# Performance work log

Measured on AMD Instinct MI355X. Metric: run time of the kernel, lower is better.

## Reference

```python
import jax, jax.numpy as jnp
import numpy as np

B, TQ, TK = 8, 256, 256
DQ, DK, DV, H = 512, 512, 512, 256


def setup_inputs() -> dict:
    key = jax.random.key(0)
    k1, k2, k3, k4, k5, k6 = jax.random.split(key, 6)
    queries = jax.random.normal(k1, (B, TQ, DQ), dtype=jnp.float32)
    keys = jax.random.normal(k2, (B, TK, DK), dtype=jnp.float32)
    values = jax.random.normal(k3, (B, TK, DV), dtype=jnp.float32)
    # Linear(in, out, bias=False): y = x @ W.T with W (out,in); store transposed (in,out)
    Wq = jax.random.normal(k4, (DQ, H), dtype=jnp.float32) / np.sqrt(DQ)
    Wk = jax.random.normal(k5, (DK, H), dtype=jnp.float32) / np.sqrt(DK)
    wv = jax.random.normal(k6, (H,), dtype=jnp.float32) / np.sqrt(H)
    return {"queries": queries, "keys": keys, "values": values,
            "Wq": Wq, "Wk": Wk, "wv": wv}


def reference(queries, keys, values, Wq, Wk, wv):
    q = jnp.einsum('bqd,dh->bqh', queries, Wq)          # (B,Tq,H)
    k = jnp.einsum('bkd,dh->bkh', keys, Wk)             # (B,Tk,H)
    features = jnp.tanh(q[:, :, None, :] + k[:, None, :, :])  # (B,Tq,Tk,H)
    scores = jnp.einsum('bqkh,h->bqk', features, wv)    # (B,Tq,Tk)
    attn = jax.nn.softmax(scores, axis=-1)              # (B,Tq,Tk)
    return jnp.einsum('bqk,bkv->bqv', attn, values)     # (B,Tq,Dv)
```

## Files before the change

### kernel.cpp

```cpp
#include <hip/hip_runtime.h>

typedef float v2f __attribute__((ext_vector_type(2)));
typedef short bf16x8 __attribute__((ext_vector_type(8)));
typedef float f32x4 __attribute__((ext_vector_type(4)));

namespace {
constexpr int B   = 8;
constexpr int TQ  = 256;
constexpr int TK  = 256;
constexpr int DQK = 512;
constexpr int DV  = 512;
constexpr int H   = 256;
constexpr int QB  = 4;
constexpr float C2LOG2E   = 2.8853900817779268f;
constexpr float NEG2LOG2E = -2.8853900817779268f;
}

__device__ __forceinline__ uint32_t f2u(float x) { return __builtin_bit_cast(uint32_t, x); }
__device__ __forceinline__ float u2f(uint32_t x) { return __builtin_bit_cast(float, x); }
__device__ __forceinline__ uint32_t pack_hi(float x, float y) {
    return (f2u(y) & 0xFFFF0000u) | (f2u(x) >> 16);
}

__global__ __launch_bounds__(256)
void proj_kernel(const float* __restrict__ Q, const float* __restrict__ Kin,
                 const float* __restrict__ Wq, const float* __restrict__ Wk,
                 float* __restrict__ qpc, float* __restrict__ kpc4)
{
    __shared__ short Ahi[4][64][8];
    __shared__ short Alo[4][64][8];
    __shared__ short Bhi[4][32][8];
    __shared__ short Blo[4][32][8];

    const bool kside = (blockIdx.z == 1);
    const float* A = kside ? Kin : Q;
    const float* W = kside ? Wk  : Wq;
    const int m0 = blockIdx.x * 64;
    const int n0 = blockIdx.y * 32;
    const int tid = threadIdx.x;

    const int am = tid >> 2, ag = tid & 3;
    const int bk = tid >> 3, bn4 = (tid & 7) * 4;
    const float4* aptr = (const float4*)(A + (m0 + am) * DQK) + ag * 2;
    const float*  wptr = W + bk * H + n0 + bn4;

    const int w = tid >> 6, l = tid & 63;
    const int wm = (w >> 1) * 32, wn = (w & 1) * 16;
    const int fg = l >> 4;
    const int fr = l & 15;

    float4 a0 = aptr[0], a1 = aptr[1];
    float4 bv = *(const float4*)wptr;

    f32x4 acc0 = {0.f, 0.f, 0.f, 0.f};
    f32x4 acc1 = {0.f, 0.f, 0.f, 0.f};

    for (int s = 0; s < 16; ++s) {
        __syncthreads();
        {
            float ah0 = u2f(f2u(a0.x) & 0xFFFF0000u), ah1 = u2f(f2u(a0.y) & 0xFFFF0000u);
            float ah2 = u2f(f2u(a0.z) & 0xFFFF0000u), ah3 = u2f(f2u(a0.w) & 0xFFFF0000u);
            float ah4 = u2f(f2u(a1.x) & 0xFFFF0000u), ah5 = u2f(f2u(a1.y) & 0xFFFF0000u);
            float ah6 = u2f(f2u(a1.z) & 0xFFFF0000u), ah7 = u2f(f2u(a1.w) & 0xFFFF0000u);
            int4 hw, lw;
            hw.x = (int)pack_hi(a0.x, a0.y); hw.y = (int)pack_hi(a0.z, a0.w);
            hw.z = (int)pack_hi(a1.x, a1.y); hw.w = (int)pack_hi(a1.z, a1.w);
            lw.x = (int)pack_hi(a0.x - ah0, a0.y - ah1);
            lw.y = (int)pack_hi(a0.z - ah2, a0.w - ah3);
            lw.z = (int)pack_hi(a1.x - ah4, a1.y - ah5);
            lw.w = (int)pack_hi(a1.z - ah6, a1.w - ah7);
            *(int4*)&Ahi[ag][am][0] = hw;
            *(int4*)&Alo[ag][am][0] = lw;
            const int g = bk >> 3, slot = bk & 7;
            float bb[4] = {bv.x, bv.y, bv.z, bv.w};
            #pragma unroll
            for (int i = 0; i < 4; ++i) {
                uint32_t u = f2u(bb[i]);
                float hf = u2f(u & 0xFFFF0000u);
                Bhi[g][bn4 + i][slot] = (short)(u >> 16);
                Blo[g][bn4 + i][slot] = (short)(f2u(bb[i] - hf) >> 16);
            }
        }
        __syncthreads();
        if (s < 15) {
            a0 = aptr[s * 8 + 8];
            a1 = aptr[s * 8 + 9];
            bv = *(const float4*)(wptr + (s + 1) * 32 * H);
        }
        bf16x8 ah_0 = *(const bf16x8*)&Ahi[fg][wm + fr][0];
        bf16x8 ah_1 = *(const bf16x8*)&Ahi[fg][wm + 16 + fr][0];
        bf16x8 al_0 = *(const bf16x8*)&Alo[fg][wm + fr][0];
        bf16x8 al_1 = *(const bf16x8*)&Alo[fg][wm + 16 + fr][0];
        bf16x8 bh   = *(const bf16x8*)&Bhi[fg][wn + fr][0];
        bf16x8 bl   = *(const bf16x8*)&Blo[fg][wn + fr][0];
        acc0 = __builtin_amdgcn_mfma_f32_16x16x32_bf16(ah_0, bh, acc0, 0, 0, 0);
        acc1 = __builtin_amdgcn_mfma_f32_16x16x32_bf16(ah_1, bh, acc1, 0, 0, 0);
        acc0 = __builtin_amdgcn_mfma_f32_16x16x32_bf16(ah_0, bl, acc0, 0, 0, 0);
        acc1 = __builtin_amdgcn_mfma_f32_16x16x32_bf16(ah_1, bl, acc1, 0, 0, 0);
        acc0 = __builtin_amdgcn_mfma_f32_16x16x32_bf16(al_0, bh, acc0, 0, 0, 0);
        acc1 = __builtin_amdgcn_mfma_f32_16x16x32_bf16(al_1, bh, acc1, 0, 0, 0);
    }

    const int col = n0 + wn + fr;
    #pragma unroll
    for (int mi = 0; mi < 2; ++mi) {
        f32x4 acc = mi ? acc1 : acc0;
        #pragma unroll
        for (int r = 0; r < 4; ++r) {
            const int row = m0 + wm + mi * 16 + fg * 4 + r;
            float val = __builtin_amdgcn_exp2f(acc[r] * C2LOG2E);
            if (!kside) {
                qpc[row * H + col] = val;
            } else {
                const int bb2 = row >> 8, kk = row & 255;
                kpc4[((bb2 * (H / 4) + (col >> 2)) * TK + kk) * 4 + (col & 3)] = val;
            }
        }
    }
}

__global__ __launch_bounds__(512, 8)
void attn_kernel(const float* __restrict__ qpc, const float* __restrict__ kpc4,
                 const float* __restrict__ wv, const float* __restrict__ values,
                 float* __restrict__ opart, float* __restrict__ rs_g)
{
    __shared__ float qlds[H][QB];
    __shared__ float wlds[H];
    __shared__ float accbuf[8][QB][128];
    __shared__ float pT[128][QB];

    const int bid = blockIdx.x;
    const int b   = bid >> 7;
    const int qg  = (bid >> 1) & 63;
    const int kh  = bid & 1;
    const int q0  = qg * QB;
    const int tid = threadIdx.x;

    for (int i = tid; i < QB * H; i += 512) {
        const int h = i >> 2, q = i & 3;
        qlds[h][q] = qpc[(b * TQ + q0 + q) * H + h];
    }
    if (tid < H) wlds[tid] = wv[tid];
    __syncthreads();

    {
        const int kp = tid & 63;
        const int hg = tid >> 6;
        const int h0 = hg * 32;
        const float4* kc = (const float4*)kpc4 + (b * (H / 4) + hg * 8) * TK
                           + (kh * 128 + 2 * kp);
        v2f a01a = {0.f, 0.f}, a23a = {0.f, 0.f};
        v2f a01b = {0.f, 0.f}, a23b = {0.f, 0.f};
        float4 kva4 = kc[0];
        float4 kvb4 = kc[1];
        #pragma unroll
        for (int h4 = 0; h4 < 8; ++h4) {
            float4 nkva, nkvb;
            if (h4 < 7) {
                nkva = kc[(h4 + 1) * TK];
                nkvb = kc[(h4 + 1) * TK + 1];
            }
            float4 w4 = *(const float4*)&wlds[h0 + h4 * 4];
            #pragma unroll
            for (int j = 0; j < 4; ++j) {
                const int h = h0 + h4 * 4 + j;
                const float ea = (j == 0) ? kva4.x : (j == 1) ? kva4.y : (j == 2) ? kva4.z : kva4.w;
                const float eb = (j == 0) ? kvb4.x : (j == 1) ? kvb4.y : (j == 2) ? kvb4.z : kvb4.w;
                const float wj = (j == 0) ? w4.x  : (j == 1) ? w4.y  : (j == 2) ? w4.z  : w4.w;
                float4 qa = *(const float4*)&qlds[h][0];
                v2f q01 = {qa.x, qa.y}, q23 = {qa.z, qa.w};
                v2f ea2 = {ea, ea}, eb2 = {eb, eb}, w2 = {wj, wj};
                v2f one = {1.0f, 1.0f};
                v2f d0a = __builtin_elementwise_fma(q01, ea2, one);
                v2f d1a = __builtin_elementwise_fma(q23, ea2, one);
                v2f d0b = __builtin_elementwise_fma(q01, eb2, one);
                v2f d1b = __builtin_elementwise_fma(q23, eb2, one);
                v2f r0a, r1a, r0b, r1b;
                r0a.x = __builtin_amdgcn_rcpf(d0a.x);
                r0a.y = __builtin_amdgcn_rcpf(d0a.y);
                r1a.x = __builtin_amdgcn_rcpf(d1a.x);
                r1a.y = __builtin_amdgcn_rcpf(d1a.y);
                r0b.x = __builtin_amdgcn_rcpf(d0b.x);
                r0b.y = __builtin_amdgcn_rcpf(d0b.y);
                r1b.x = __builtin_amdgcn_rcpf(d1b.x);
                r1b.y = __builtin_amdgcn_rcpf(d1b.y);
                a01a = __builtin_elementwise_fma(w2, r0a, a01a);
                a23a = __builtin_elementwise_fma(w2, r1a, a23a);
                a01b = __builtin_elementwise_fma(w2, r0b, a01b);
                a23b = __builtin_elementwise_fma(w2, r1b, a23b);
            }
            kva4 = nkva;
            kvb4 = nkvb;
        }
        accbuf[hg][0][2 * kp]     = a01a.x;
        accbuf[hg][1][2 * kp]     = a01a.y;
        accbuf[hg][2][2 * kp]     = a23a.x;
        accbuf[hg][3][2 * kp]     = a23a.y;
        accbuf[hg][0][2 * kp + 1] = a01b.x;
        accbuf[hg][1][2 * kp + 1] = a01b.y;
        accbuf[hg][2][2 * kp + 1] = a23b.x;
        accbuf[hg][3][2 * kp + 1] = a23b.y;
    }
    __syncthreads();

    {
        const int q = tid >> 7, kl = tid & 127;
        float s = ((accbuf[0][q][kl] + accbuf[1][q][kl]) +
                   (accbuf[2][q][kl] + accbuf[3][q][kl])) +
                  ((accbuf[4][q][kl] + accbuf[5][q][kl]) +
                   (accbuf[6][q][kl] + accbuf[7][q][kl]));
        pT[kl][q] = __builtin_amdgcn_exp2f(s * NEG2LOG2E);
    }
    __syncthreads();

    {
        const int wave = tid >> 6, lane = tid & 63;
        if (wave < QB) {
            float s = pT[lane][wave] + pT[lane + 64][wave];
            #pragma unroll
            for (int off = 1; off < 64; off <<= 1)
                s += __shfl_xor(s, off);
            if (lane == 0) rs_g[(b * TQ + q0 + wave) * 2 + kh] = s;
        }
    }

    {
        const int c = tid;
        const float* vb = values + (b * TK + kh * 128) * DV + c;
        v2f o01 = {0.f, 0.f}, o23 = {0.f, 0.f};
        #pragma unroll 8
        for (int kk = 0; kk < 128; ++kk) {
            float v = vb[kk * DV];
            float4 p4 = *(const float4*)&pT[kk][0];
            v2f vv = {v, v};
            v2f p01 = {p4.x, p4.y}, p23 = {p4.z, p4.w};
            o01 = __builtin_elementwise_fma(p01, vv, o01);
            o23 = __builtin_elementwise_fma(p23, vv, o23);
        }
        float* ob = opart + kh * (B * TQ * DV) + (b * TQ + q0) * DV + c;
        ob[0 * DV] = o01.x;
        ob[1 * DV] = o01.y;
        ob[2 * DV] = o23.x;
        ob[3 * DV] = o23.y;
    }
}

__global__ __launch_bounds__(256)
void epilogue_kernel(const float* __restrict__ opart, const float* __restrict__ rs_g,
                     float* __restrict__ out)
{
    const int idx4 = blockIdx.x * 256 + threadIdx.x;
    const int row  = idx4 >> 7;
    float rs = rs_g[2 * row] + rs_g[2 * row + 1];
    float inv = __builtin_amdgcn_rcpf(rs);
    const float4* o0 = (const float4*)opart;
    const float4* o1 = (const float4*)(opart + B * TQ * DV);
    float4 a = o0[idx4], bq = o1[idx4];
    float4 r;
    r.x = (a.x + bq.x) * inv;
    r.y = (a.y + bq.y) * inv;
    r.z = (a.z + bq.z) * inv;
    r.w = (a.w + bq.w) * inv;
    ((float4*)out)[idx4] = r;
}

extern "C" void kernel_launch(void* const* d_in, const int* in_sizes, int n_in,
                              void* d_out, int out_size, void* d_ws, size_t ws_size,
                              hipStream_t stream)
{
    const float* queries = (const float*)d_in[0];
    const float* keys    = (const float*)d_in[1];
    const float* values  = (const float*)d_in[2];
    const float* Wq      = (const float*)d_in[3];
    const float* Wk      = (const float*)d_in[4];
    const float* wv      = (const float*)d_in[5];
    float* out   = (float*)d_out;
    float* qpc   = (float*)d_ws;
    float* kpc4  = qpc + B * TQ * H;
    float* opart = kpc4 + B * H * TK;
    float* rs_g  = opart + 2 * B * TQ * DV;

    dim3 gproj(B * TQ / 64, H / 32, 2);
    proj_kernel<<<gproj, 256, 0, stream>>>(queries, keys, Wq, Wk, qpc, kpc4);
    attn_kernel<<<B * (TQ / QB) * 2, 512, 0, stream>>>(qpc, kpc4, wv, values, opart, rs_g);
    epilogue_kernel<<<B * TQ * DV / 4 / 256, 256, 0, stream>>>(opart, rs_g, out);
}
```

Measured before the change: 49.83 us.

## Process eight queries per attention block to increase key and value reuse

Doubles the query tile per block from four to eight, so each loaded key feature and value element is used for twice as many queries. The score loop is reorganised so each thread handles one key across eight queries over 64 hidden units, with four hidden-unit groups instead of eight. This halves global traffic for keys and values per query and the number of blocks. In exchange it raises register use and lowers the launch-bounds occupancy hint from 8 to 4 blocks.

Result: no change. 49.04 us (-1.6%).

```diff
diff --git a/kernel.cpp b/kernel.cpp
--- a/kernel.cpp
+++ b/kernel.cpp
@@ -11,7 +11,7 @@
 constexpr int DQK = 512;
 constexpr int DV  = 512;
 constexpr int H   = 256;
-constexpr int QB  = 4;
+constexpr int QB  = 8;
 constexpr float C2LOG2E   = 2.8853900817779268f;
 constexpr float NEG2LOG2E = -2.8853900817779268f;
 }
@@ -119,129 +119,128 @@
     }
 }
 
-__global__ __launch_bounds__(512, 8)
+__global__ __launch_bounds__(512, 4)
 void attn_kernel(const float* __restrict__ qpc, const float* __restrict__ kpc4,
                  const float* __restrict__ wv, const float* __restrict__ values,
                  float* __restrict__ opart, float* __restrict__ rs_g)
 {
     __shared__ float qlds[H][QB];
     __shared__ float wlds[H];
-    __shared__ float accbuf[8][QB][128];
+    __shared__ float accbuf[4][QB][128];
     __shared__ float pT[128][QB];
 
     const int bid = blockIdx.x;
-    const int b   = bid >> 7;
-    const int qg  = (bid >> 1) & 63;
+    const int b   = bid >> 6;
+    const int qg  = (bid >> 1) & 31;
     const int kh  = bid & 1;
     const int q0  = qg * QB;
     const int tid = threadIdx.x;
 
     for (int i = tid; i < QB * H; i += 512) {
-        const int h = i >> 2, q = i & 3;
+        const int h = i >> 3, q = i & 7;
         qlds[h][q] = qpc[(b * TQ + q0 + q) * H + h];
     }
     if (tid < H) wlds[tid] = wv[tid];
     __syncthreads();
 
     {
-        const int kp = tid & 63;
-        const int hg = tid >> 6;
-        const int h0 = hg * 32;
-        const float4* kc = (const float4*)kpc4 + (b * (H / 4) + hg * 8) * TK
-                           + (kh * 128 + 2 * kp);
-        v2f a01a = {0.f, 0.f}, a23a = {0.f, 0.f};
-        v2f a01b = {0.f, 0.f}, a23b = {0.f, 0.f};
-        float4 kva4 = kc[0];
-        float4 kvb4 = kc[1];
+        const int kp = tid & 127;
+        const int hg = tid >> 7;
+        const int h0 = hg * 64;
+        const float4* kc = (const float4*)kpc4 + (b * (H / 4) + hg * 16) * TK
+                           + (kh * 128 + kp);
+        v2f a01 = {0.f, 0.f}, a23 = {0.f, 0.f};
+        v2f a45 = {0.f, 0.f}, a67 = {0.f, 0.f};
+        const v2f one = {1.0f, 1.0f};
+        float4 kv = kc[0];
         #pragma unroll
-        for (int h4 = 0; h4 < 8; ++h4) {
-            float4 nkva, nkvb;
-            if (h4 < 7) {
-                nkva = kc[(h4 + 1) * TK];
-                nkvb = kc[(h4 + 1) * TK + 1];
-            }
+        for (int h4 = 0; h4 < 16; ++h4) {
+            float4 nkv;
+            if (h4 < 15) nkv = kc[(h4 + 1) * TK];
             float4 w4 = *(const float4*)&wlds[h0 + h4 * 4];
             #pragma unroll
             for (int j = 0; j < 4; ++j) {
                 const int h = h0 + h4 * 4 + j;
-                const float ea = (j == 0) ? kva4.x : (j == 1) ? kva4.y : (j == 2) ? kva4.z : kva4.w;
-                const float eb = (j == 0) ? kvb4.x : (j == 1) ? kvb4.y : (j == 2) ? kvb4.z : kvb4.w;
-                const float wj = (j == 0) ? w4.x  : (j == 1) ? w4.y  : (j == 2) ? w4.z  : w4.w;
+                const float ek = (j == 0) ? kv.x : (j == 1) ? kv.y : (j == 2) ? kv.z : kv.w;
+                const float wj = (j == 0) ? w4.x : (j == 1) ? w4.y : (j == 2) ? w4.z : w4.w;
                 float4 qa = *(const float4*)&qlds[h][0];
-                v2f q01 = {qa.x, qa.y}, q23 = {qa.z, qa.w};
-                v2f ea2 = {ea, ea}, eb2 = {eb, eb}, w2 = {wj, wj};
-                v2f one = {1.0f, 1.0f};
-                v2f d0a = __builtin_elementwise_fma(q01, ea2, one);
-                v2f d1a = __builtin_elementwise_fma(q23, ea2, one);
-                v2f d0b = __builtin_elementwise_fma(q01, eb2, one);
-                v2f d1b = __builtin_elementwise_fma(q23, eb2, one);
-                v2f r0a, r1a, r0b, r1b;
-                r0a.x = __builtin_amdgcn_rcpf(d0a.x);
-                r0a.y = __builtin_amdgcn_rcpf(d0a.y);
-                r1a.x = __builtin_amdgcn_rcpf(d1a.x);
-                r1a.y = __builtin_amdgcn_rcpf(d1a.y);
-                r0b.x = __builtin_amdgcn_rcpf(d0b.x);
-                r0b.y = __builtin_amdgcn_rcpf(d0b.y);
-                r1b.x = __builtin_amdgcn_rcpf(d1b.x);
-                r1b.y = __builtin_amdgcn_rcpf(d1b.y);
-                a01a = __builtin_elementwise_fma(w2, r0a, a01a);
-                a23a = __builtin_elementwise_fma(w2, r1a, a23a);
-                a01b = __builtin_elementwise_fma(w2, r0b, a01b);
-                a23b = __builtin_elementwise_fma(w2, r1b, a23b);
+                float4 qb = *(const float4*)&qlds[h][4];
+                v2f ek2 = {ek, ek}, w2 = {wj, wj};
+                v2f qp0 = {qa.x, qa.y}, qp1 = {qa.z, qa.w};
+                v2f qp2 = {qb.x, qb.y}, qp3 = {qb.z, qb.w};
+                v2f d0 = __builtin_elementwise_fma(qp0, ek2, one);
+                v2f d1 = __builtin_elementwise_fma(qp1, ek2, one);
+                v2f d2 = __builtin_elementwise_fma(qp2, ek2, one);
+                v2f d3 = __builtin_elementwise_fma(qp3, ek2, one);
+                v2f r0, r1, r2, r3;
+                r0.x = __builtin_amdgcn_rcpf(d0.x);
+                r0.y = __builtin_amdgcn_rcpf(d0.y);
+                r1.x = __builtin_amdgcn_rcpf(d1.x);
+                r1.y = __builtin_amdgcn_rcpf(d1.y);
+                r2.x = __builtin_amdgcn_rcpf(d2.x);
+                r2.y = __builtin_amdgcn_rcpf(d2.y);
+                r3.x = __builtin_amdgcn_rcpf(d3.x);
+                r3.y = __builtin_amdgcn_rcpf(d3.y);
+                a01 = __builtin_elementwise_fma(w2, r0, a01);
+                a23 = __builtin_elementwise_fma(w2, r1, a23);
+                a45 = __builtin_elementwise_fma(w2, r2, a45);
+                a67 = __builtin_elementwise_fma(w2, r3, a67);
             }
-            kva4 = nkva;
-            kvb4 = nkvb;
-        }
-        accbuf[hg][0][2 * kp]     = a01a.x;
-        accbuf[hg][1][2 * kp]     = a01a.y;
-        accbuf[hg][2][2 * kp]     = a23a.x;
-        accbuf[hg][3][2 * kp]     = a23a.y;
-        accbuf[hg][0][2 * kp + 1] = a01b.x;
-        accbuf[hg][1][2 * kp + 1] = a01b.y;
-        accbuf[hg][2][2 * kp + 1] = a23b.x;
-        accbuf[hg][3][2 * kp + 1] = a23b.y;
+            kv = nkv;
+        }
+        accbuf[hg][0][kp] = a01.x;
+        accbuf[hg][1][kp] = a01.y;
+        accbuf[hg][2][kp] = a23.x;
+        accbuf[hg][3][kp] = a23.y;
+        accbuf[hg][4][kp] = a45.x;
+        accbuf[hg][5][kp] = a45.y;
+        accbuf[hg][6][kp] = a67.x;
+        accbuf[hg][7][kp] = a67.y;
     }
     __syncthreads();
 
-    {
-        const int q = tid >> 7, kl = tid & 127;
-        float s = ((accbuf[0][q][kl] + accbuf[1][q][kl]) +
-                   (accbuf[2][q][kl] + accbuf[3][q][kl])) +
-                  ((accbuf[4][q][kl] + accbuf[5][q][kl]) +
-                   (accbuf[6][q][kl] + accbuf[7][q][kl]));
+    for (int i = tid; i < QB * 128; i += 512) {
+        const int q = i >> 7, kl = i & 127;
+        float s = (accbuf[0][q][kl] + accbuf[1][q][kl]) +
+                  (accbuf[2][q][kl] + accbuf[3][q][kl]);
         pT[kl][q] = __builtin_amdgcn_exp2f(s * NEG2LOG2E);
     }
     __syncthreads();
 
     {
         const int wave = tid >> 6, lane = tid & 63;
-        if (wave < QB) {
-            float s = pT[lane][wave] + pT[lane + 64][wave];
-            #pragma unroll
-            for (int off = 1; off < 64; off <<= 1)
-                s += __shfl_xor(s, off);
-            if (lane == 0) rs_g[(b * TQ + q0 + wave) * 2 + kh] = s;
-        }
+        float s = pT[lane][wave] + pT[lane + 64][wave];
+        #pragma unroll
+        for (int off = 1; off < 64; off <<= 1)
+            s += __shfl_xor(s, off);
+        if (lane == 0) rs_g[(b * TQ + q0 + wave) * 2 + kh] = s;
     }
 
     {
         const int c = tid;
         const float* vb = values + (b * TK + kh * 128) * DV + c;
         v2f o01 = {0.f, 0.f}, o23 = {0.f, 0.f};
+        v2f o45 = {0.f, 0.f}, o67 = {0.f, 0.f};
         #pragma unroll 8
         for (int kk = 0; kk < 128; ++kk) {
             float v = vb[kk * DV];
-            float4 p4 = *(const float4*)&pT[kk][0];
+            float4 p4a = *(const float4*)&pT[kk][0];
+            float4 p4b = *(const float4*)&pT[kk][4];
             v2f vv = {v, v};
-            v2f p01 = {p4.x, p4.y}, p23 = {p4.z, p4.w};
-            o01 = __builtin_elementwise_fma(p01, vv, o01);
-            o23 = __builtin_elementwise_fma(p23, vv, o23);
+            o01 = __builtin_elementwise_fma((v2f){p4a.x, p4a.y}, vv, o01);
+            o23 = __builtin_elementwise_fma((v2f){p4a.z, p4a.w}, vv, o23);
+            o45 = __builtin_elementwise_fma((v2f){p4b.x, p4b.y}, vv, o45);
+            o67 = __builtin_elementwise_fma((v2f){p4b.z, p4b.w}, vv, o67);
         }
         float* ob = opart + kh * (B * TQ * DV) + (b * TQ + q0) * DV + c;
         ob[0 * DV] = o01.x;
         ob[1 * DV] = o01.y;
         ob[2 * DV] = o23.x;
         ob[3 * DV] = o23.y;
+        ob[4 * DV] = o45.x;
+        ob[5 * DV] = o45.y;
+        ob[6 * DV] = o67.x;
+        ob[7 * DV] = o67.y;
     }
 }
 
```
